# Optimization experiments

Measured on AMD Instinct MI355X. Metric: run time of the kernel, lower is better.

## Reference

```python
import jax, jax.numpy as jnp
import numpy as np

DIM = 768; DEPTH = 8; HEADS = 12; DH = 64; DFF = 2048
SOFTCLAMP = 50.0; TIME_EVERY = 4
B, T, S = 2, 32, 256
EPS = 1e-6


def rmsnorm(x, w):
    return x * jax.lax.rsqrt(jnp.mean(x * x, axis=-1, keepdims=True) + EPS) * w


def l2norm(x):
    n = jnp.sqrt(jnp.sum(x * x, axis=-1, keepdims=True))
    return x / jnp.maximum(n, 1e-12)


def make_rotary(n):
    inv = 1.0 / (10000.0 ** (jnp.arange(0, DH, 2, dtype=jnp.float32) / DH))
    f = jnp.arange(n, dtype=jnp.float32)[:, None] * inv[None, :]
    return jnp.concatenate([f, f], axis=-1)  # (n, DH)


def apply_rot(rot, x):
    # x: (B', H, n, DH), rot: (n, DH)
    x1, x2 = jnp.split(x, 2, axis=-1)
    return x * jnp.cos(rot) + jnp.concatenate([-x2, x1], axis=-1) * jnp.sin(rot)


def attn_block(x, rv, nw, wq, wk, wv, wo, wg, wmix, bm, kgam, rot, causal):
    # x: (B', n, DIM); rv: (B', H, n, DH) value-residual
    Bp, n, _ = x.shape
    tn = rmsnorm(x, nw)
    q = (tn @ wq).reshape(Bp, n, HEADS, DH).transpose(0, 2, 1, 3)
    k = (tn @ wk).reshape(Bp, n, HEADS, DH).transpose(0, 2, 1, 3)
    v = (tn @ wv).reshape(Bp, n, HEADS, DH).transpose(0, 2, 1, 3)
    # learned value-residual lerp: v <- v + mix * (rv - v)
    mix = jax.nn.sigmoid(tn @ wmix + bm).transpose(0, 2, 1)[..., None]
    v = v + mix * (rv - v)
    # MultiHeadRMSNorm on keys: l2norm * (gamma+1) * sqrt(DH)
    k = l2norm(k) * ((kgam + 1.0) * (DH ** 0.5))[:, None, :]
    if rot is not None:
        q = apply_rot(rot, q)
        k = apply_rot(rot, k)
    sim = jnp.einsum('bhid,bhjd->bhij', q, k) * (DH ** -0.5)
    sim = jnp.tanh(sim / SOFTCLAMP) * SOFTCLAMP
    if causal:
        cm = jnp.triu(jnp.ones((n, n), dtype=bool), 1)
        sim = jnp.where(cm, -jnp.finfo(sim.dtype).max, sim)
    attn = jax.nn.softmax(sim, axis=-1)
    o = jnp.einsum('bhij,bhjd->bhid', attn, v)
    gates = jax.nn.sigmoid(tn @ wg).transpose(0, 2, 1)[..., None]
    o = o * gates
    o = o.transpose(0, 2, 1, 3).reshape(Bp, n, HEADS * DH)
    return o @ wo


def ff_block(x, nw, win, bi, wout, bo):
    tn = rmsnorm(x, nw)
    h = tn @ win + bi
    a, g = jnp.split(h, 2, axis=-1)
    return (a * jax.nn.gelu(g, approximate=False)) @ wout + bo


def setup_inputs() -> dict:
    key = jax.random.key(0)
    ks = jax.random.split(key, 16)
    def rn(k, shape, scale=0.02):
        return jax.random.normal(k, shape, dtype=jnp.float32) * scale
    return {
        'tokens': jax.random.normal(ks[0], (B, T, S, DIM), dtype=jnp.float32),
        'attn_norm_w': jnp.ones((DEPTH, DIM), jnp.float32),
        'Wq': rn(ks[1], (DEPTH, DIM, HEADS * DH)),
        'Wk': rn(ks[2], (DEPTH, DIM, HEADS * DH)),
        'Wv': rn(ks[3], (DEPTH, DIM, HEADS * DH)),
        'Wo': rn(ks[4], (DEPTH, HEADS * DH, DIM)),
        'Wg': rn(ks[5], (DEPTH, DIM, HEADS)),
        'Wmix': rn(ks[6], (DEPTH, DIM, HEADS)),
        'bmix': jnp.zeros((DEPTH, HEADS), jnp.float32),
        'k_gamma': rn(ks[7], (DEPTH, HEADS, DH)),
        'ff_norm_w': jnp.ones((DEPTH, DIM), jnp.float32),
        'Win': rn(ks[8], (DEPTH, DIM, 2 * DFF)),
        'b_in': jnp.zeros((DEPTH, 2 * DFF), jnp.float32),
        'Wout': rn(ks[9], (DEPTH, DFF, DIM)),
        'b_out': jnp.zeros((DEPTH, DIM), jnp.float32),
        'vr_norm_w': jnp.ones((DIM,), jnp.float32),
        'vr_W': rn(ks[10], (DIM, HEADS * DH)),
        'final_norm_w': jnp.ones((DIM,), jnp.float32),
    }


def reference(tokens, attn_norm_w, Wq, Wk, Wv, Wo, Wg, Wmix, bmix, k_gamma,
              ff_norm_w, Win, b_in, Wout, b_out, vr_norm_w, vr_W, final_norm_w):
    b, t, s, d = tokens.shape
    # value residuals computed once from the input tokens
    rv = (rmsnorm(tokens, vr_norm_w) @ vr_W).reshape(b, t, s, HEADS, DH)
    rot = make_rotary(t)
    x = tokens
    for i in range(DEPTH):
        is_time = ((i + 1) % TIME_EVERY == 0)
        if is_time:
            xa = x.transpose(0, 2, 1, 3).reshape(b * s, t, d)
            rva = rv.transpose(0, 2, 3, 1, 4).reshape(b * s, HEADS, t, DH)
            o = attn_block(xa, rva, attn_norm_w[i], Wq[i], Wk[i], Wv[i], Wo[i],
                           Wg[i], Wmix[i], bmix[i], k_gamma[i], rot, True)
            o = o.reshape(b, s, t, d).transpose(0, 2, 1, 3)
        else:
            xa = x.reshape(b * t, s, d)
            rva = rv.transpose(0, 1, 3, 2, 4).reshape(b * t, HEADS, s, DH)
            o = attn_block(xa, rva, attn_norm_w[i], Wq[i], Wk[i], Wv[i], Wo[i],
                           Wg[i], Wmix[i], bmix[i], k_gamma[i], None, False)
            o = o.reshape(b, t, s, d)
        x = x + o
        x = x + ff_block(x, ff_norm_w[i], Win[i], b_in[i], Wout[i], b_out[i])
    return rmsnorm(x, final_norm_w)
```

## Files before the change

kernel.cpp:

```cpp
#include <hip/hip_runtime.h>
#include <cmath>

#define DIM 768
#define DEPTH 8
#define HEADS 12
#define DH 64
#define DFF 2048
#define NTOK 16384
#define BB 2
#define TT 32
#define SS 256
#define LDQ 2304

typedef __attribute__((ext_vector_type(8))) short short8;
typedef __attribute__((ext_vector_type(4))) float f32x4;

__device__ __forceinline__ float sigmoidf_(float x) { return 1.0f / (1.0f + __expf(-x)); }
__device__ __forceinline__ float geluf_(float x) {
  return 0.5f * x * (1.0f + erff(x * 0.70710678118654752f));
}
__device__ __forceinline__ unsigned short f2bf(float x) {
  union { float f; unsigned int u; } a; a.f = x;
  unsigned int r = a.u + 0x7fff + ((a.u >> 16) & 1);
  return (unsigned short)(r >> 16);
}
__device__ __forceinline__ float bf2f(unsigned short h) {
  union { unsigned int u; float f; } a; a.u = ((unsigned int)h) << 16;
  return a.f;
}
__device__ __forceinline__ void load_lds16(const void* g, void* l) {
  __builtin_amdgcn_global_load_lds(
      (const __attribute__((address_space(1))) unsigned int*)g,
      (__attribute__((address_space(3))) unsigned int*)l, 16, 0, 0);
}
__device__ __forceinline__ float softclamp_exp(float sv) {
  float a = exp2f(sv * 0.057707802f);
  float rc = __builtin_amdgcn_rcpf(a + 1.0f);
  return exp2f(fmaf(-144.26950408f, rc, 72.13475204f));
}

template<int BF>
__global__ __launch_bounds__(256) void rmsnorm_kernel(
    const float* __restrict__ x, const float* __restrict__ w, void* __restrict__ outp)
{
  int row = blockIdx.x;
  int tid = threadIdx.x;
  const float* xr = x + (size_t)row * DIM;
  float v0 = xr[tid], v1 = xr[tid + 256], v2 = xr[tid + 512];
  float ss = v0 * v0 + v1 * v1 + v2 * v2;
  #pragma unroll
  for (int off = 32; off; off >>= 1) ss += __shfl_xor(ss, off);
  __shared__ float sred[4];
  if ((tid & 63) == 0) sred[tid >> 6] = ss;
  __syncthreads();
  float tot = sred[0] + sred[1] + sred[2] + sred[3];
  float r = rsqrtf(tot * (1.0f / DIM) + 1e-6f);
  if (BF) {
    unsigned short* orow = (unsigned short*)outp + (size_t)row * DIM;
    orow[tid]       = f2bf(v0 * r * w[tid]);
    orow[tid + 256] = f2bf(v1 * r * w[tid + 256]);
    orow[tid + 512] = f2bf(v2 * r * w[tid + 512]);
  } else {
    float* orow = (float*)outp + (size_t)row * DIM;
    orow[tid]       = v0 * r * w[tid];
    orow[tid + 256] = v1 * r * w[tid + 256];
    orow[tid + 512] = v2 * r * w[tid + 512];
  }
}

__global__ __launch_bounds__(256) void w_to_bt(
    const float* __restrict__ W, unsigned short* __restrict__ WT, int K, int N)
{
  __shared__ float t[32][33];
  int n0 = blockIdx.x * 32, k0 = blockIdx.y * 32;
  int c = threadIdx.x & 31, r8 = threadIdx.x >> 5;
  #pragma unroll
  for (int rr = r8; rr < 32; rr += 8)
    t[rr][c] = W[(size_t)(k0 + rr) * N + n0 + c];
  __syncthreads();
  #pragma unroll
  for (int rn = r8; rn < 32; rn += 8)
    WT[(size_t)(n0 + rn) * K + k0 + c] = f2bf(t[c][rn]);
}

template<int MODE>
__global__ __launch_bounds__(256) void gemm_bf16(
    const unsigned short* __restrict__ A, const unsigned short* __restrict__ BT,
    float* __restrict__ Cf, unsigned short* __restrict__ Hg,
    const float* __restrict__ bias, int M, int N, int K)
{
  __shared__ unsigned short As[128 * 32];
  __shared__ unsigned short Bs[128 * 32];
  const int tid = threadIdx.x;
  const int wave = tid >> 6;
  const int lane = tid & 63;
  const int bm = blockIdx.y * 128;
  const int bn = blockIdx.x * 128;
  const int wm = (wave & 1) * 64;
  const int wn = (wave >> 1) * 64;

  f32x4 acc[4][4];
  #pragma unroll
  for (int i = 0; i < 4; ++i)
    #pragma unroll
    for (int j = 0; j < 4; ++j) acc[i][j] = (f32x4){0.f, 0.f, 0.f, 0.f};

  const int srow = wave * 32 + (lane >> 2);
  const int skoff = (lane & 3) * 8;
  const unsigned short* gA = A + (size_t)(bm + srow) * K + skoff;
  const unsigned short* gB = BT + (size_t)(bn + srow) * K + skoff;
  unsigned short* lA = &As[(wave * 32) * 32];
  unsigned short* lB = &Bs[(wave * 32) * 32];

  const int fr = lane & 15;
  const int fq = (lane >> 4) * 8;

  for (int k0 = 0; k0 < K; k0 += 32) {
    load_lds16(gA + k0, lA);
    load_lds16(gA + k0 + 16 * K, lA + 16 * 32);
    load_lds16(gB + k0, lB);
    load_lds16(gB + k0 + 16 * K, lB + 16 * 32);
    __syncthreads();
    short8 a[4], b[4];
    #pragma unroll
    for (int i = 0; i < 4; ++i)
      a[i] = *(const short8*)&As[(wm + 16 * i + fr) * 32 + fq];
    #pragma unroll
    for (int j = 0; j < 4; ++j)
      b[j] = *(const short8*)&Bs[(wn + 16 * j + fr) * 32 + fq];
    #pragma unroll
    for (int i = 0; i < 4; ++i)
      #pragma unroll
      for (int j = 0; j < 4; ++j)
        acc[i][j] = __builtin_amdgcn_mfma_f32_16x16x32_bf16(a[i], b[j], acc[i][j], 0, 0, 0);
    __syncthreads();
  }

  const int crow0 = bm + wm + (lane >> 4) * 4;
  const int ccol0 = bn + wn + fr;
  float bv[4];
  #pragma unroll
  for (int j = 0; j < 4; ++j) bv[j] = bias ? bias[ccol0 + 16 * j] : 0.0f;
  #pragma unroll
  for (int i = 0; i < 4; ++i) {
    #pragma unroll
    for (int r = 0; r < 4; ++r) {
      int row = crow0 + 16 * i + r;
      #pragma unroll
      for (int j = 0; j < 4; ++j) {
        int col = ccol0 + 16 * j;
        size_t idx = (size_t)row * N + col;
        float val = acc[i][j][r] + bv[j];
        if (MODE == 0) Cf[idx] = val;
        else if (MODE == 1) Cf[idx] += val;
        else Hg[idx] = f2bf(val);
      }
    }
  }
}

__global__ __launch_bounds__(256, 2) void gemm_ff(
    const unsigned short* __restrict__ A, const unsigned short* __restrict__ BTa,
    const unsigned short* __restrict__ BTg, unsigned short* __restrict__ Hg,
    const float* __restrict__ ba, const float* __restrict__ bg, int M, int N, int K)
{
  __shared__ unsigned short As[128 * 32];
  __shared__ unsigned short Bas[128 * 32];
  __shared__ unsigned short Bgs[128 * 32];
  const int tid = threadIdx.x;
  const int wave = tid >> 6;
  const int lane = tid & 63;
  const int bm = blockIdx.y * 128;
  const int bn = blockIdx.x * 128;
  const int wm = (wave & 1) * 64;
  const int wn = (wave >> 1) * 64;

  f32x4 acca[4][4], accg[4][4];
  #pragma unroll
  for (int i = 0; i < 4; ++i)
    #pragma unroll
    for (int j = 0; j < 4; ++j) {
      acca[i][j] = (f32x4){0.f, 0.f, 0.f, 0.f};
      accg[i][j] = (f32x4){0.f, 0.f, 0.f, 0.f};
    }

  const int srow = wave * 32 + (lane >> 2);
  const int skoff = (lane & 3) * 8;
  const unsigned short* gA  = A   + (size_t)(bm + srow) * K + skoff;
  const unsigned short* gBa = BTa + (size_t)(bn + srow) * K + skoff;
  const unsigned short* gBg = BTg + (size_t)(bn + srow) * K + skoff;
  unsigned short* lA  = &As[(wave * 32) * 32];
  unsigned short* lBa = &Bas[(wave * 32) * 32];
  unsigned short* lBg = &Bgs[(wave * 32) * 32];

  const int fr = lane & 15;
  const int fq = (lane >> 4) * 8;

  for (int k0 = 0; k0 < K; k0 += 32) {
    load_lds16(gA + k0, lA);
    load_lds16(gA + k0 + 16 * K, lA + 16 * 32);
    load_lds16(gBa + k0, lBa);
    load_lds16(gBa + k0 + 16 * K, lBa + 16 * 32);
    load_lds16(gBg + k0, lBg);
    load_lds16(gBg + k0 + 16 * K, lBg + 16 * 32);
    __syncthreads();
    short8 a[4], b1[4], b2[4];
    #pragma unroll
    for (int i = 0; i < 4; ++i)
      a[i] = *(const short8*)&As[(wm + 16 * i + fr) * 32 + fq];
    #pragma unroll
    for (int j = 0; j < 4; ++j) {
      b1[j] = *(const short8*)&Bas[(wn + 16 * j + fr) * 32 + fq];
      b2[j] = *(const short8*)&Bgs[(wn + 16 * j + fr) * 32 + fq];
    }
    #pragma unroll
    for (int i = 0; i < 4; ++i)
      #pragma unroll
      for (int j = 0; j < 4; ++j) {
        acca[i][j] = __builtin_amdgcn_mfma_f32_16x16x32_bf16(a[i], b1[j], acca[i][j], 0, 0, 0);
        accg[i][j] = __builtin_amdgcn_mfma_f32_16x16x32_bf16(a[i], b2[j], accg[i][j], 0, 0, 0);
      }
    __syncthreads();
  }

  const int crow0 = bm + wm + (lane >> 4) * 4;
  const int ccol0 = bn + wn + fr;
  float bva[4], bvg[4];
  #pragma unroll
  for (int j = 0; j < 4; ++j) {
    bva[j] = ba[ccol0 + 16 * j];
    bvg[j] = bg[ccol0 + 16 * j];
  }
  #pragma unroll
  for (int i = 0; i < 4; ++i) {
    #pragma unroll
    for (int r = 0; r < 4; ++r) {
      int row = crow0 + 16 * i + r;
      #pragma unroll
      for (int j = 0; j < 4; ++j) {
        int col = ccol0 + 16 * j;
        float av = acca[i][j][r] + bva[j];
        float gv = accg[i][j][r] + bvg[j];
        Hg[(size_t)row * N + col] = f2bf(av * geluf_(gv));
      }
    }
  }
}

__global__ __launch_bounds__(256) void proj12x2_kernel(
    const unsigned short* __restrict__ A, const float* __restrict__ Bw1,
    const float* __restrict__ b1, const float* __restrict__ Bw2,
    float* __restrict__ out1, float* __restrict__ out2)
{
  int row = blockIdx.x * 4 + (threadIdx.x >> 6);
  int lane = threadIdx.x & 63;
  const unsigned short* ar = A + (size_t)row * DIM;
  float acc1[HEADS], acc2[HEADS];
  #pragma unroll
  for (int j = 0; j < HEADS; ++j) { acc1[j] = 0.0f; acc2[j] = 0.0f; }
  for (int k2 = lane; k2 < DIM; k2 += 64) {
    float a = bf2f(ar[k2]);
    const float* bw1 = Bw1 + (size_t)k2 * HEADS;
    const float* bw2 = Bw2 + (size_t)k2 * HEADS;
    #pragma unroll
    for (int j = 0; j < HEADS; ++j) {
      acc1[j] = fmaf(a, bw1[j], acc1[j]);
      acc2[j] = fmaf(a, bw2[j], acc2[j]);
    }
  }
  #pragma unroll
  for (int j = 0; j < HEADS; ++j) {
    #pragma unroll
    for (int off = 32; off; off >>= 1) {
      acc1[j] += __shfl_xor(acc1[j], off);
      acc2[j] += __shfl_xor(acc2[j], off);
    }
  }
  if (lane < HEADS) {
    out1[(size_t)row * HEADS + lane] = sigmoidf_(acc1[lane] + b1[lane]);
    out2[(size_t)row * HEADS + lane] = sigmoidf_(acc2[lane]);
  }
}

__global__ __launch_bounds__(768) void qkv_fix_kernel(
    unsigned short* __restrict__ qkv, const unsigned short* __restrict__ rvb,
    const float* __restrict__ mix, const float* __restrict__ kgam, int is_time)
{
  int tok = blockIdx.x;
  int h = threadIdx.x >> 6;
  int d = threadIdx.x & 63;
  size_t rowb = (size_t)tok * LDQ + h * DH + d;
  float kv = bf2f(qkv[rowb + 768]);
  float ss = kv * kv;
  #pragma unroll
  for (int off = 32; off; off >>= 1) ss += __shfl_xor(ss, off);
  float nrm = fmaxf(sqrtf(ss), 1e-12f);
  kv = kv / nrm * (kgam[h * DH + d] + 1.0f) * 8.0f;
  float mv = mix[(size_t)tok * HEADS + h];
  float vv = bf2f(qkv[rowb + 1536]);
  float rvv = bf2f(rvb[(size_t)tok * DIM + h * DH + d]);
  qkv[rowb + 1536] = f2bf(vv + mv * (rvv - vv));
  float qv = bf2f(qkv[rowb]);
  if (is_time) {
    int t = (tok >> 8) & 31;
    int j = d & 31;
    float ang = (float)t * __expf(-(float)j * (9.210340371976184f / 32.0f));
    float cs = cosf(ang), sn = sinf(ang);
    float qp = __shfl_xor(qv, 32);
    float kp = __shfl_xor(kv, 32);
    float sgn = (d < 32) ? -1.0f : 1.0f;
    qv = qv * cs + sgn * qp * sn;
    kv = kv * cs + sgn * kp * sn;
  }
  qkv[rowb] = f2bf(qv);
  qkv[rowb + 768] = f2bf(kv);
}

__global__ __launch_bounds__(256, 3) void attn_mfma_kernel(
    const unsigned short* __restrict__ q, const unsigned short* __restrict__ k,
    const unsigned short* __restrict__ v, const float* __restrict__ gate,
    unsigned short* __restrict__ o)
{
  __shared__ __align__(16) unsigned short Ks[128 * 64];
  __shared__ __align__(16) unsigned short VsT[64 * 128];
  __shared__ __align__(16) unsigned short Pw[4][32 * 64];
  const int tid = threadIdx.x;
  const int wave = tid >> 6;
  const int lane = tid & 63;
  const int g = lane >> 4;
  const int c16 = lane & 15;
  const int bp = blockIdx.x >> 1;
  const int qh = blockIdx.x & 1;
  const int h = blockIdx.y;
  const size_t qoff = (size_t)bp * SS * LDQ + h * DH;
  const int qbase = qh * 128 + wave * 32;

  short8 aq[2][2];
  #pragma unroll
  for (int i = 0; i < 2; ++i) {
    const unsigned short* qp = q + qoff + (size_t)(qbase + i * 16 + c16) * LDQ;
    #pragma unroll
    for (int cc = 0; cc < 2; ++cc)
      aq[i][cc] = *(const short8*)(qp + cc * 32 + g * 8);
  }

  f32x4 oacc[2][4];
  float rs[2][4];
  #pragma unroll
  for (int i = 0; i < 2; ++i)
    #pragma unroll
    for (int j = 0; j < 4; ++j) {
      oacc[i][j] = (f32x4){0.f, 0.f, 0.f, 0.f};
      rs[i][j] = 0.f;
    }

  const int srow_ = tid >> 3;
  const int su_ = tid & 7;

  for (int half = 0; half < 2; ++half) {
    const int r0 = half * 128;
    #pragma unroll
    for (int it = 0; it < 4; ++it) {
      int row = srow_ + it * 32;
      const unsigned short* src =
          k + qoff + (size_t)(r0 + row) * LDQ + ((su_ ^ (row & 7)) << 3);
      load_lds16(src, &Ks[(wave * 64 + it * 2048 / 8) * 8]);
    }
    #pragma unroll
    for (int it = 0; it < 4; ++it) {
      int f = tid + it * 256;
      int j = f & 127, dq = f >> 7;
      short8 t = *(const short8*)(v + qoff + (size_t)(r0 + j) * LDQ + dq * 8);
      int u = j >> 3;
      #pragma unroll
      for (int c = 0; c < 8; ++c) {
        int d = dq * 8 + c;
        VsT[d * 128 + ((u ^ (d & 15)) << 3) + (j & 7)] = (unsigned short)t[c];
      }
    }
    __syncthreads();

    #pragma unroll
    for (int jc = 0; jc < 2; ++jc) {
      const int lr0 = jc * 64;
      f32x4 s[2][4];
      #pragma unroll
      for (int i = 0; i < 2; ++i)
        #pragma unroll
        for (int j = 0; j < 4; ++j) s[i][j] = (f32x4){0.f, 0.f, 0.f, 0.f};
      #pragma unroll
      for (int jt = 0; jt < 4; ++jt) {
        int row = lr0 + jt * 16 + c16;
        short8 b0 = *(const short8*)&Ks[row * 64 + ((g ^ (row & 7)) << 3)];
        short8 b1 = *(const short8*)&Ks[row * 64 + (((4 + g) ^ (row & 7)) << 3)];
        #pragma unroll
        for (int i = 0; i < 2; ++i) {
          s[i][jt] = __builtin_amdgcn_mfma_f32_16x16x32_bf16(aq[i][0], b0, s[i][jt], 0, 0, 0);
          s[i][jt] = __builtin_amdgcn_mfma_f32_16x16x32_bf16(aq[i][1], b1, s[i][jt], 0, 0, 0);
        }
      }
      #pragma unroll
      for (int i = 0; i < 2; ++i) {
        #pragma unroll
        for (int jt = 0; jt < 4; ++jt) {
          int pj = jt * 16 + c16;
          int uj = pj >> 3;
          #pragma unroll
          for (int r = 0; r < 4; ++r) {
            float p = softclamp_exp(s[i][jt][r] * 0.125f);
            unsigned short pb = f2bf(p);
            rs[i][r] += bf2f(pb);
            int prow = i * 16 + g * 4 + r;
            Pw[wave][prow * 64 + ((uj ^ (prow & 7)) << 3) + (pj & 7)] = pb;
          }
        }
      }
      #pragma unroll
      for (int jj = 0; jj < 2; ++jj) {
        short8 pa[2];
        #pragma unroll
        for (int i = 0; i < 2; ++i) {
          int prow = i * 16 + c16;
          int u = jj * 4 + g;
          pa[i] = *(const short8*)&Pw[wave][prow * 64 + ((u ^ (prow & 7)) << 3)];
        }
        const int jl = lr0 + jj * 32 + g * 8;
        const int uv = jl >> 3;
        #pragma unroll
        for (int dt = 0; dt < 4; ++dt) {
          int d = dt * 16 + c16;
          short8 bv = *(const short8*)&VsT[d * 128 + ((uv ^ (d & 15)) << 3)];
          #pragma unroll
          for (int i = 0; i < 2; ++i)
            oacc[i][dt] = __builtin_amdgcn_mfma_f32_16x16x32_bf16(pa[i], bv, oacc[i][dt], 0, 0, 0);
        }
      }
    }
    __syncthreads();
  }

  #pragma unroll
  for (int i = 0; i < 2; ++i)
    #pragma unroll
    for (int r = 0; r < 4; ++r) {
      float t = rs[i][r];
      t += __shfl_xor(t, 1); t += __shfl_xor(t, 2);
      t += __shfl_xor(t, 4); t += __shfl_xor(t, 8);
      rs[i][r] = t;
    }
  #pragma unroll
  for (int i = 0; i < 2; ++i) {
    #pragma unroll
    for (int r = 0; r < 4; ++r) {
      int row = qbase + i * 16 + g * 4 + r;
      int tq = bp * SS + row;
      float gt = gate[(size_t)tq * HEADS + h] / rs[i][r];
      unsigned short* op = o + (size_t)tq * DIM + h * DH;
      #pragma unroll
      for (int dt = 0; dt < 4; ++dt)
        op[dt * 16 + c16] = f2bf(oacc[i][dt][r] * gt);
    }
  }
}

__global__ __launch_bounds__(256, 3) void attn_time_mfma(
    const unsigned short* __restrict__ q, const unsigned short* __restrict__ k,
    const unsigned short* __restrict__ v, const float* __restrict__ gate,
    unsigned short* __restrict__ o)
{
  __shared__ __align__(16) unsigned short VT[4][64 * 32];
  __shared__ __align__(16) unsigned short Pw[4][32 * 32];
  const int tid = threadIdx.x;
  const int wave = tid >> 6;
  const int lane = tid & 63;
  const int g = lane >> 4;
  const int c16 = lane & 15;
  const int h = blockIdx.y;
  const int sp = blockIdx.x * 4 + wave;
  const int base = (sp >> 8) * (TT * SS) + (sp & 255);

  short8 aq[2][2], bk[2][2];
  #pragma unroll
  for (int i = 0; i < 2; ++i) {
    const unsigned short* qp = q + (size_t)(base + (i * 16 + c16) * SS) * LDQ + h * DH;
    const unsigned short* kp = k + (size_t)(base + (i * 16 + c16) * SS) * LDQ + h * DH;
    #pragma unroll
    for (int cc = 0; cc < 2; ++cc) {
      aq[i][cc] = *(const short8*)(qp + cc * 32 + g * 8);
      bk[i][cc] = *(const short8*)(kp + cc * 32 + g * 8);
    }
  }

  {
    int tp = lane >> 1;
    int dh0 = (lane & 1) * 32;
    const unsigned short* vp = v + (size_t)(base + tp * SS) * LDQ + h * DH + dh0;
    int ut = tp >> 3;
    #pragma unroll
    for (int j4 = 0; j4 < 4; ++j4) {
      short8 t = *(const short8*)(vp + j4 * 8);
      #pragma unroll
      for (int c = 0; c < 8; ++c) {
        int d = dh0 + j4 * 8 + c;
        VT[wave][d * 32 + ((ut ^ (d & 3)) << 3) + (tp & 7)] = (unsigned short)t[c];
      }
    }
  }

  f32x4 s[2][2];
  #pragma unroll
  for (int i = 0; i < 2; ++i)
    #pragma unroll
    for (int j = 0; j < 2; ++j) s[i][j] = (f32x4){0.f, 0.f, 0.f, 0.f};
  #pragma unroll
  for (int jt = 0; jt < 2; ++jt)
    #pragma unroll
    for (int i = 0; i < 2; ++i) {
      s[i][jt] = __builtin_amdgcn_mfma_f32_16x16x32_bf16(aq[i][0], bk[jt][0], s[i][jt], 0, 0, 0);
      s[i][jt] = __builtin_amdgcn_mfma_f32_16x16x32_bf16(aq[i][1], bk[jt][1], s[i][jt], 0, 0, 0);
    }

  float rs[2][4];
  #pragma unroll
  for (int i = 0; i < 2; ++i)
    #pragma unroll
    for (int r = 0; r < 4; ++r) rs[i][r] = 0.f;
  #pragma unroll
  for (int i = 0; i < 2; ++i) {
    #pragma unroll
    for (int jt = 0; jt < 2; ++jt) {
      int pj = jt * 16 + c16;
      int uj = pj >> 3;
      #pragma unroll
      for (int r = 0; r < 4; ++r) {
        int t = i * 16 + g * 4 + r;
        float p = softclamp_exp(s[i][jt][r] * 0.125f);
        unsigned short pb = (pj <= t) ? f2bf(p) : (unsigned short)0;
        rs[i][r] += bf2f(pb);
        Pw[wave][t * 32 + ((uj ^ (t & 3)) << 3) + (pj & 7)] = pb;
      }
    }
  }

  short8 pa[2];
  #pragma unroll
  for (int i = 0; i < 2; ++i) {
    int prow = i * 16 + c16;
    pa[i] = *(const short8*)&Pw[wave][prow * 32 + ((g ^ (prow & 3)) << 3)];
  }
  f32x4 oacc[2][4];
  #pragma unroll
  for (int dt = 0; dt < 4; ++dt) {
    int d = dt * 16 + c16;
    short8 bv = *(const short8*)&VT[wave][d * 32 + ((g ^ (d & 3)) << 3)];
    #pragma unroll
    for (int i = 0; i < 2; ++i)
      oacc[i][dt] = __builtin_amdgcn_mfma_f32_16x16x32_bf16(
          pa[i], bv, (f32x4){0.f, 0.f, 0.f, 0.f}, 0, 0, 0);
  }

  #pragma unroll
  for (int i = 0; i < 2; ++i)
    #pragma unroll
    for (int r = 0; r < 4; ++r) {
      float t = rs[i][r];
      t += __shfl_xor(t, 1); t += __shfl_xor(t, 2);
      t += __shfl_xor(t, 4); t += __shfl_xor(t, 8);
      rs[i][r] = t;
    }
  #pragma unroll
  for (int i = 0; i < 2; ++i) {
    #pragma unroll
    for (int r = 0; r < 4; ++r) {
      int t = i * 16 + g * 4 + r;
      int tok = base + t * SS;
      float gt = gate[(size_t)tok * HEADS + h] / rs[i][r];
      unsigned short* op = o + (size_t)tok * DIM + h * DH;
      #pragma unroll
      for (int dt = 0; dt < 4; ++dt)
        op[dt * 16 + c16] = f2bf(oacc[i][dt][r] * gt);
    }
  }
}

extern "C" void kernel_launch(void* const* d_in, const int* in_sizes, int n_in,
                              void* d_out, int out_size, void* d_ws, size_t ws_size,
                              hipStream_t stream)
{
  const float* tokens = (const float*)d_in[0];
  const float* attn_norm_w = (const float*)d_in[1];
  const float* Wq   = (const float*)d_in[2];
  const float* Wk   = (const float*)d_in[3];
  const float* Wv   = (const float*)d_in[4];
  const float* Wo   = (const float*)d_in[5];
  const float* Wg   = (const float*)d_in[6];
  const float* Wmix = (const float*)d_in[7];
  const float* bmix = (const float*)d_in[8];
  const float* kgam = (const float*)d_in[9];
  const float* ffw  = (const float*)d_in[10];
  const float* Win  = (const float*)d_in[11];
  const float* bin  = (const float*)d_in[12];
  const float* Wout = (const float*)d_in[13];
  const float* bout = (const float*)d_in[14];
  const float* vrw  = (const float*)d_in[15];
  const float* vrW  = (const float*)d_in[16];
  const float* fnw  = (const float*)d_in[17];

  const size_t NT = (size_t)NTOK * DIM;
  float* ws  = (float*)d_ws;
  float* x   = ws;
  float* mix = x + NT;
  float* gate = mix + (size_t)NTOK * HEADS;
  unsigned short* tn   = (unsigned short*)(gate + (size_t)NTOK * HEADS);
  unsigned short* qkv  = tn + NT;
  unsigned short* rvb  = qkv + (size_t)NTOK * LDQ;
  unsigned short* wqkvT = rvb + NT;
  unsigned short* woT  = wqkvT + (size_t)2304 * 768;
  unsigned short* winT = woT + (size_t)768 * 768;
  unsigned short* woutT= winT + (size_t)4096 * 768;
  unsigned short* vrWT = woutT + (size_t)768 * 2048;
  unsigned short* hg   = qkv;

  hipMemcpyAsync(x, tokens, NT * sizeof(float), hipMemcpyDeviceToDevice, stream);

  w_to_bt<<<dim3(24, 24), 256, 0, stream>>>(vrW, vrWT, DIM, DIM);
  rmsnorm_kernel<1><<<NTOK, 256, 0, stream>>>(tokens, vrw, tn);
  gemm_bf16<2><<<dim3(6, 128), 256, 0, stream>>>(
      tn, vrWT, nullptr, rvb, nullptr, NTOK, DIM, DIM);

  for (int i = 0; i < DEPTH; ++i) {
    int is_time = ((i + 1) % 4 == 0) ? 1 : 0;
    w_to_bt<<<dim3(24, 24), 256, 0, stream>>>(Wq + (size_t)i * DIM * DIM, wqkvT, DIM, DIM);
    w_to_bt<<<dim3(24, 24), 256, 0, stream>>>(Wk + (size_t)i * DIM * DIM, wqkvT + (size_t)768 * 768, DIM, DIM);
    w_to_bt<<<dim3(24, 24), 256, 0, stream>>>(Wv + (size_t)i * DIM * DIM, wqkvT + (size_t)1536 * 768, DIM, DIM);
    w_to_bt<<<dim3(24, 24), 256, 0, stream>>>(Wo + (size_t)i * DIM * DIM, woT, DIM, DIM);
    w_to_bt<<<dim3(128, 24), 256, 0, stream>>>(Win + (size_t)i * DIM * 2 * DFF, winT, DIM, 2 * DFF);
    w_to_bt<<<dim3(24, 64), 256, 0, stream>>>(Wout + (size_t)i * DFF * DIM, woutT, DFF, DIM);

    rmsnorm_kernel<1><<<NTOK, 256, 0, stream>>>(x, attn_norm_w + (size_t)i * DIM, tn);
    gemm_bf16<2><<<dim3(18, 128), 256, 0, stream>>>(
        tn, wqkvT, nullptr, qkv, nullptr, NTOK, LDQ, DIM);
    proj12x2_kernel<<<NTOK / 4, 256, 0, stream>>>(
        tn, Wmix + (size_t)i * DIM * HEADS, bmix + (size_t)i * HEADS,
        Wg + (size_t)i * DIM * HEADS, mix, gate);
    qkv_fix_kernel<<<dim3(NTOK), 768, 0, stream>>>(
        qkv, rvb, mix, kgam + (size_t)i * HEADS * DH, is_time);
    if (is_time)
      attn_time_mfma<<<dim3((BB * SS) / 4, HEADS), 256, 0, stream>>>(
          qkv, qkv + 768, qkv + 1536, gate, tn);
    else
      attn_mfma_kernel<<<dim3(BB * TT * 2, HEADS), 256, 0, stream>>>(
          qkv, qkv + 768, qkv + 1536, gate, tn);
    gemm_bf16<1><<<dim3(6, 128), 256, 0, stream>>>(tn, woT, x, nullptr, nullptr, NTOK, DIM, DIM);
    rmsnorm_kernel<1><<<NTOK, 256, 0, stream>>>(x, ffw + (size_t)i * DIM, tn);
    gemm_ff<<<dim3(16, 128), 256, 0, stream>>>(
        tn, winT, winT + (size_t)DFF * DIM, hg,
        bin + (size_t)i * 2 * DFF, bin + (size_t)i * 2 * DFF + DFF, NTOK, DFF, DIM);
    gemm_bf16<1><<<dim3(6, 128), 256, 0, stream>>>(
        hg, woutT, x, nullptr, bout + (size_t)i * DIM, NTOK, DIM, DFF);
  }
  rmsnorm_kernel<0><<<NTOK, 256, 0, stream>>>(x, fnw, (float*)d_out);
}
```

Measured before the change: 5.030 ms.

## Fuse weight conversions, interleave GLU weights, fold qkv fix into spatial attention

The six per-layer weight transpose launches become one kernel, and that kernel interleaves the Win columns in 16-wide chunks so that value and gate columns sit next to each other. The FF up-projection then runs through the generic gemm_bf16 with a new GLU epilogue mode instead of the dual-accumulator gemm_ff. For non-time layers, the key l2norm/gamma scaling and the value-residual lerp now happen inside the attention kernel's LDS staging, which drops the separate qkv_fix pass and its reads and writes of qkv. The costs are a longer attention prologue and the loss of the async LDS load for K. The GEMM also changes shape: a doubled grid with half the accumulators per block.

```diff
diff --git a/kernel.cpp b/kernel.cpp
--- a/kernel.cpp
+++ b/kernel.cpp
@@ -83,6 +83,45 @@
     WT[(size_t)(n0 + rn) * K + k0 + c] = f2bf(t[c][rn]);
 }
 
+__global__ __launch_bounds__(256) void w_convert_layer(
+    const float* __restrict__ Wq, const float* __restrict__ Wk,
+    const float* __restrict__ Wv, const float* __restrict__ Wo,
+    const float* __restrict__ Win, const float* __restrict__ Wout,
+    unsigned short* __restrict__ wqkvT, unsigned short* __restrict__ woT,
+    unsigned short* __restrict__ winT, unsigned short* __restrict__ woutT)
+{
+  __shared__ float tle[32][33];
+  int t = blockIdx.x;
+  const float* W; unsigned short* WT; int K, N, n0, k0, glu = 0;
+  if (t < 1728) {
+    int rg = t / 576, tt = t - rg * 576;
+    W = (rg == 0) ? Wq : (rg == 1) ? Wk : Wv;
+    WT = wqkvT + (size_t)rg * 768 * 768;
+    K = 768; N = 768; n0 = (tt % 24) * 32; k0 = (tt / 24) * 32;
+  } else if (t < 2304) {
+    int tt = t - 1728; W = Wo; WT = woT;
+    K = 768; N = 768; n0 = (tt % 24) * 32; k0 = (tt / 24) * 32;
+  } else if (t < 5376) {
+    int tt = t - 2304; W = Win; WT = winT;
+    K = 768; N = 4096; n0 = (tt % 128) * 32; k0 = (tt / 128) * 32; glu = 1;
+  } else {
+    int tt = t - 5376; W = Wout; WT = woutT;
+    K = 2048; N = 768; n0 = (tt % 24) * 32; k0 = (tt / 24) * 32;
+  }
+  int c = threadIdx.x & 31, r8 = threadIdx.x >> 5;
+  int col = n0 + c;
+  int scol = col;
+  if (glu) {
+    int b = col >> 5, rr2 = col & 31;
+    scol = (rr2 < 16) ? (b * 16 + rr2) : (2048 + b * 16 + rr2 - 16);
+  }
+  for (int rr = r8; rr < 32; rr += 8)
+    tle[rr][c] = W[(size_t)(k0 + rr) * N + scol];
+  __syncthreads();
+  for (int rn = r8; rn < 32; rn += 8)
+    WT[(size_t)(n0 + rn) * K + k0 + c] = f2bf(tle[c][rn]);
+}
+
 template<int MODE>
 __global__ __launch_bounds__(256) void gemm_bf16(
     const unsigned short* __restrict__ A, const unsigned short* __restrict__ BT,
@@ -139,109 +178,33 @@
   const int crow0 = bm + wm + (lane >> 4) * 4;
   const int ccol0 = bn + wn + fr;
   float bv[4];
-  #pragma unroll
-  for (int j = 0; j < 4; ++j) bv[j] = bias ? bias[ccol0 + 16 * j] : 0.0f;
+  if (MODE != 3) {
+    #pragma unroll
+    for (int j = 0; j < 4; ++j) bv[j] = bias ? bias[ccol0 + 16 * j] : 0.0f;
+  }
   #pragma unroll
   for (int i = 0; i < 4; ++i) {
     #pragma unroll
     for (int r = 0; r < 4; ++r) {
       int row = crow0 + 16 * i + r;
-      #pragma unroll
-      for (int j = 0; j < 4; ++j) {
-        int col = ccol0 + 16 * j;
-        size_t idx = (size_t)row * N + col;
-        float val = acc[i][j][r] + bv[j];
-        if (MODE == 0) Cf[idx] = val;
-        else if (MODE == 1) Cf[idx] += val;
-        else Hg[idx] = f2bf(val);
-      }
-    }
-  }
-}
-
-__global__ __launch_bounds__(256, 2) void gemm_ff(
-    const unsigned short* __restrict__ A, const unsigned short* __restrict__ BTa,
-    const unsigned short* __restrict__ BTg, unsigned short* __restrict__ Hg,
-    const float* __restrict__ ba, const float* __restrict__ bg, int M, int N, int K)
-{
-  __shared__ unsigned short As[128 * 32];
-  __shared__ unsigned short Bas[128 * 32];
-  __shared__ unsigned short Bgs[128 * 32];
-  const int tid = threadIdx.x;
-  const int wave = tid >> 6;
-  const int lane = tid & 63;
-  const int bm = blockIdx.y * 128;
-  const int bn = blockIdx.x * 128;
-  const int wm = (wave & 1) * 64;
-  const int wn = (wave >> 1) * 64;
-
-  f32x4 acca[4][4], accg[4][4];
-  #pragma unroll
-  for (int i = 0; i < 4; ++i)
-    #pragma unroll
-    for (int j = 0; j < 4; ++j) {
-      acca[i][j] = (f32x4){0.f, 0.f, 0.f, 0.f};
-      accg[i][j] = (f32x4){0.f, 0.f, 0.f, 0.f};
-    }
-
-  const int srow = wave * 32 + (lane >> 2);
-  const int skoff = (lane & 3) * 8;
-  const unsigned short* gA  = A   + (size_t)(bm + srow) * K + skoff;
-  const unsigned short* gBa = BTa + (size_t)(bn + srow) * K + skoff;
-  const unsigned short* gBg = BTg + (size_t)(bn + srow) * K + skoff;
-  unsigned short* lA  = &As[(wave * 32) * 32];
-  unsigned short* lBa = &Bas[(wave * 32) * 32];
-  unsigned short* lBg = &Bgs[(wave * 32) * 32];
-
-  const int fr = lane & 15;
-  const int fq = (lane >> 4) * 8;
-
-  for (int k0 = 0; k0 < K; k0 += 32) {
-    load_lds16(gA + k0, lA);
-    load_lds16(gA + k0 + 16 * K, lA + 16 * 32);
-    load_lds16(gBa + k0, lBa);
-    load_lds16(gBa + k0 + 16 * K, lBa + 16 * 32);
-    load_lds16(gBg + k0, lBg);
-    load_lds16(gBg + k0 + 16 * K, lBg + 16 * 32);
-    __syncthreads();
-    short8 a[4], b1[4], b2[4];
-    #pragma unroll
-    for (int i = 0; i < 4; ++i)
-      a[i] = *(const short8*)&As[(wm + 16 * i + fr) * 32 + fq];
-    #pragma unroll
-    for (int j = 0; j < 4; ++j) {
-      b1[j] = *(const short8*)&Bas[(wn + 16 * j + fr) * 32 + fq];
-      b2[j] = *(const short8*)&Bgs[(wn + 16 * j + fr) * 32 + fq];
-    }
-    #pragma unroll
-    for (int i = 0; i < 4; ++i)
-      #pragma unroll
-      for (int j = 0; j < 4; ++j) {
-        acca[i][j] = __builtin_amdgcn_mfma_f32_16x16x32_bf16(a[i], b1[j], acca[i][j], 0, 0, 0);
-        accg[i][j] = __builtin_amdgcn_mfma_f32_16x16x32_bf16(a[i], b2[j], accg[i][j], 0, 0, 0);
-      }
-    __syncthreads();
-  }
-
-  const int crow0 = bm + wm + (lane >> 4) * 4;
-  const int ccol0 = bn + wn + fr;
-  float bva[4], bvg[4];
-  #pragma unroll
-  for (int j = 0; j < 4; ++j) {
-    bva[j] = ba[ccol0 + 16 * j];
-    bvg[j] = bg[ccol0 + 16 * j];
-  }
-  #pragma unroll
-  for (int i = 0; i < 4; ++i) {
-    #pragma unroll
-    for (int r = 0; r < 4; ++r) {
-      int row = crow0 + 16 * i + r;
-      #pragma unroll
-      for (int j = 0; j < 4; ++j) {
-        int col = ccol0 + 16 * j;
-        float av = acca[i][j][r] + bva[j];
-        float gv = accg[i][j][r] + bvg[j];
-        Hg[(size_t)row * N + col] = f2bf(av * geluf_(gv));
+      if (MODE == 3) {
+        #pragma unroll
+        for (int pj = 0; pj < 2; ++pj) {
+          int b32 = (bn + wn + 32 * pj) >> 5;
+          float av = acc[i][2 * pj][r] + bias[b32 * 16 + fr];
+          float gv = acc[i][2 * pj + 1][r] + bias[2048 + b32 * 16 + fr];
+          Hg[(size_t)row * (N >> 1) + b32 * 16 + fr] = f2bf(av * geluf_(gv));
+        }
+      } else {
+        #pragma unroll
+        for (int j = 0; j < 4; ++j) {
+          int col = ccol0 + 16 * j;
+          size_t idx = (size_t)row * N + col;
+          float val = acc[i][j][r] + bv[j];
+          if (MODE == 0) Cf[idx] = val;
+          else if (MODE == 1) Cf[idx] += val;
+          else Hg[idx] = f2bf(val);
+        }
       }
     }
   }
@@ -318,8 +281,9 @@
 
 __global__ __launch_bounds__(256, 3) void attn_mfma_kernel(
     const unsigned short* __restrict__ q, const unsigned short* __restrict__ k,
-    const unsigned short* __restrict__ v, const float* __restrict__ gate,
-    unsigned short* __restrict__ o)
+    const unsigned short* __restrict__ v, const unsigned short* __restrict__ rvb,
+    const float* __restrict__ mix, const float* __restrict__ gate,
+    const float* __restrict__ kgam, unsigned short* __restrict__ o)
 {
   __shared__ __align__(16) unsigned short Ks[128 * 64];
   __shared__ __align__(16) unsigned short VsT[64 * 128];
@@ -354,28 +318,47 @@
       rs[i][j] = 0.f;
     }
 
-  const int srow_ = tid >> 3;
-  const int su_ = tid & 7;
-
   for (int half = 0; half < 2; ++half) {
     const int r0 = half * 128;
     #pragma unroll
     for (int it = 0; it < 4; ++it) {
-      int row = srow_ + it * 32;
-      const unsigned short* src =
-          k + qoff + (size_t)(r0 + row) * LDQ + ((su_ ^ (row & 7)) << 3);
-      load_lds16(src, &Ks[(wave * 64 + it * 2048 / 8) * 8]);
+      int f = tid + it * 256;
+      int row = f >> 3, u = f & 7;
+      short8 t8 = *(const short8*)(k + qoff + (size_t)(r0 + row) * LDQ + u * 8);
+      float kv[8];
+      float ss = 0.f;
+      #pragma unroll
+      for (int c = 0; c < 8; ++c) { kv[c] = bf2f((unsigned short)t8[c]); ss += kv[c] * kv[c]; }
+      ss += __shfl_xor(ss, 1); ss += __shfl_xor(ss, 2); ss += __shfl_xor(ss, 4);
+      float inv = 8.0f / fmaxf(sqrtf(ss), 1e-12f);
+      float4 kg0 = *(const float4*)(kgam + h * DH + u * 8);
+      float4 kg1 = *(const float4*)(kgam + h * DH + u * 8 + 4);
+      short8 o8;
+      o8[0] = (short)f2bf(kv[0] * inv * (kg0.x + 1.0f));
+      o8[1] = (short)f2bf(kv[1] * inv * (kg0.y + 1.0f));
+      o8[2] = (short)f2bf(kv[2] * inv * (kg0.z + 1.0f));
+      o8[3] = (short)f2bf(kv[3] * inv * (kg0.w + 1.0f));
+      o8[4] = (short)f2bf(kv[4] * inv * (kg1.x + 1.0f));
+      o8[5] = (short)f2bf(kv[5] * inv * (kg1.y + 1.0f));
+      o8[6] = (short)f2bf(kv[6] * inv * (kg1.z + 1.0f));
+      o8[7] = (short)f2bf(kv[7] * inv * (kg1.w + 1.0f));
+      *(short8*)&Ks[row * 64 + ((u ^ (row & 7)) << 3)] = o8;
     }
     #pragma unroll
     for (int it = 0; it < 4; ++it) {
       int f = tid + it * 256;
       int j = f & 127, dq = f >> 7;
-      short8 t = *(const short8*)(v + qoff + (size_t)(r0 + j) * LDQ + dq * 8);
+      int tok = bp * SS + r0 + j;
+      short8 v8 = *(const short8*)(v + qoff + (size_t)(r0 + j) * LDQ + dq * 8);
+      short8 r8 = *(const short8*)(rvb + (size_t)tok * DIM + h * DH + dq * 8);
+      float mv = mix[(size_t)tok * HEADS + h];
       int u = j >> 3;
       #pragma unroll
       for (int c = 0; c < 8; ++c) {
         int d = dq * 8 + c;
-        VsT[d * 128 + ((u ^ (d & 15)) << 3) + (j & 7)] = (unsigned short)t[c];
+        float vv = bf2f((unsigned short)v8[c]);
+        float val = vv + mv * (bf2f((unsigned short)r8[c]) - vv);
+        VsT[d * 128 + ((u ^ (d & 15)) << 3) + (j & 7)] = f2bf(val);
       }
     }
     __syncthreads();
@@ -630,12 +613,11 @@
 
   for (int i = 0; i < DEPTH; ++i) {
     int is_time = ((i + 1) % 4 == 0) ? 1 : 0;
-    w_to_bt<<<dim3(24, 24), 256, 0, stream>>>(Wq + (size_t)i * DIM * DIM, wqkvT, DIM, DIM);
-    w_to_bt<<<dim3(24, 24), 256, 0, stream>>>(Wk + (size_t)i * DIM * DIM, wqkvT + (size_t)768 * 768, DIM, DIM);
-    w_to_bt<<<dim3(24, 24), 256, 0, stream>>>(Wv + (size_t)i * DIM * DIM, wqkvT + (size_t)1536 * 768, DIM, DIM);
-    w_to_bt<<<dim3(24, 24), 256, 0, stream>>>(Wo + (size_t)i * DIM * DIM, woT, DIM, DIM);
-    w_to_bt<<<dim3(128, 24), 256, 0, stream>>>(Win + (size_t)i * DIM * 2 * DFF, winT, DIM, 2 * DFF);
-    w_to_bt<<<dim3(24, 64), 256, 0, stream>>>(Wout + (size_t)i * DFF * DIM, woutT, DFF, DIM);
+    w_convert_layer<<<6912, 256, 0, stream>>>(
+        Wq + (size_t)i * DIM * DIM, Wk + (size_t)i * DIM * DIM,
+        Wv + (size_t)i * DIM * DIM, Wo + (size_t)i * DIM * DIM,
+        Win + (size_t)i * DIM * 2 * DFF, Wout + (size_t)i * DFF * DIM,
+        wqkvT, woT, winT, woutT);
 
     rmsnorm_kernel<1><<<NTOK, 256, 0, stream>>>(x, attn_norm_w + (size_t)i * DIM, tn);
     gemm_bf16<2><<<dim3(18, 128), 256, 0, stream>>>(
@@ -643,19 +625,20 @@
     proj12x2_kernel<<<NTOK / 4, 256, 0, stream>>>(
         tn, Wmix + (size_t)i * DIM * HEADS, bmix + (size_t)i * HEADS,
         Wg + (size_t)i * DIM * HEADS, mix, gate);
-    qkv_fix_kernel<<<dim3(NTOK), 768, 0, stream>>>(
-        qkv, rvb, mix, kgam + (size_t)i * HEADS * DH, is_time);
-    if (is_time)
+    if (is_time) {
+      qkv_fix_kernel<<<dim3(NTOK), 768, 0, stream>>>(
+          qkv, rvb, mix, kgam + (size_t)i * HEADS * DH, is_time);
       attn_time_mfma<<<dim3((BB * SS) / 4, HEADS), 256, 0, stream>>>(
           qkv, qkv + 768, qkv + 1536, gate, tn);
-    else
+    } else {
       attn_mfma_kernel<<<dim3(BB * TT * 2, HEADS), 256, 0, stream>>>(
-          qkv, qkv + 768, qkv + 1536, gate, tn);
+          qkv, qkv + 768, qkv + 1536, rvb, mix, gate,
+          kgam + (size_t)i * HEADS * DH, tn);
+    }
     gemm_bf16<1><<<dim3(6, 128), 256, 0, stream>>>(tn, woT, x, nullptr, nullptr, NTOK, DIM, DIM);
     rmsnorm_kernel<1><<<NTOK, 256, 0, stream>>>(x, ffw + (size_t)i * DIM, tn);
-    gemm_ff<<<dim3(16, 128), 256, 0, stream>>>(
-        tn, winT, winT + (size_t)DFF * DIM, hg,
-        bin + (size_t)i * 2 * DFF, bin + (size_t)i * 2 * DFF + DFF, NTOK, DFF, DIM);
+    gemm_bf16<3><<<dim3(32, 128), 256, 0, stream>>>(
+        tn, winT, nullptr, hg, bin + (size_t)i * 2 * DFF, NTOK, 2 * DFF, DIM);
     gemm_bf16<1><<<dim3(6, 128), 256, 0, stream>>>(
         hg, woutT, x, nullptr, bout + (size_t)i * DIM, NTOK, DIM, DFF);
   }
```

Measured after the change: 5.135 ms. 1.02x slower.
